# Optimization experiments

Measured on AMD Instinct MI355X. Metric: run time of the kernel, lower is better.

## Reference

```python
import jax, jax.numpy as jnp
import numpy as np
import math

D_MODEL = 1024
N_HEADS = 16
D_K = D_MODEL // N_HEADS


def setup_inputs() -> dict:
    key = jax.random.key(0)
    ks = jax.random.split(key, 5)
    std = math.sqrt(2.0 / (D_MODEL + D_MODEL))
    x = jax.random.normal(ks[0], (2, 2048, D_MODEL), dtype=jnp.float32)
    W_q = jax.random.normal(ks[1], (D_MODEL, D_MODEL), dtype=jnp.float32) * std
    W_k = jax.random.normal(ks[2], (D_MODEL, D_MODEL), dtype=jnp.float32) * std
    W_v = jax.random.normal(ks[3], (D_MODEL, D_MODEL), dtype=jnp.float32) * std
    W_o = jax.random.normal(ks[4], (D_MODEL, D_MODEL), dtype=jnp.float32) * std
    return {"x": x, "W_q": W_q, "W_k": W_k, "W_v": W_v, "W_o": W_o}


def reference(x, W_q, W_k, W_v, W_o):
    B, S, D = x.shape
    H, dk = N_HEADS, D_K
    # projections: (B,S,D) @ (D,D)
    def split_heads(t):  # (B,S,D) -> (B,H,S,dk)
        return t.reshape(B, S, H, dk).transpose(0, 2, 1, 3)
    Q = split_heads(x @ W_q)
    K = split_heads(x @ W_k)
    V = split_heads(x @ W_v)
    scale = 1.0 / math.sqrt(dk)
    scores = jnp.einsum("bhqd,bhkd->bhqk", Q, K) * scale  # (B,H,S,S)
    attn = jax.nn.softmax(scores, axis=-1)
    out = jnp.einsum("bhqk,bhkd->bhqd", attn, V)  # (B,H,S,dk)
    concat = out.transpose(0, 2, 1, 3).reshape(B, S, D)
    return concat @ W_o
```

## Files before the change

kernel.cpp:

```cpp
#include <hip/hip_runtime.h>
#include <hip/hip_bf16.h>
#include <math.h>

#define DMODEL 1024
#define NHEADS 16
#define DKH    64
#define BATCH  2
#define SEQ    2048
#define MROWS  (BATCH * SEQ)
#define LOG2E  1.4426950408889634f

typedef __bf16 bf16_t;
typedef bf16_t bf16x8 __attribute__((ext_vector_type(8)));
typedef bf16_t bf16x4 __attribute__((ext_vector_type(4)));
typedef float  floatx4 __attribute__((ext_vector_type(4)));

__device__ __forceinline__ void glds16(const bf16_t* g, bf16_t* l) {
    __builtin_amdgcn_global_load_lds((__attribute__((address_space(1))) unsigned*)(g),
                                     (__attribute__((address_space(3))) unsigned*)(l),
                                     16, 0, 0);
}

__global__ void prep_kernel(const float* __restrict__ x,
                            const float* __restrict__ W0, const float* __restrict__ W1,
                            const float* __restrict__ W2, const float* __restrict__ W3,
                            bf16_t* __restrict__ xb, bf16_t* __restrict__ Wt) {
    __shared__ float t[32][33];
    int bx = blockIdx.x, by = blockIdx.y, z = blockIdx.z;
    int tx = threadIdx.x, ty = threadIdx.y;
    if (z == 0) {
#pragma unroll
        for (int k = 0; k < 16; ++k) {
            int row = by * 128 + k * 8 + ty;
            int col = bx * 32 + tx;
            xb[(size_t)row * DMODEL + col] = (bf16_t)x[(size_t)row * DMODEL + col];
        }
        return;
    }
    const float* W = (z == 1) ? W0 : (z == 2) ? W1 : (z == 3) ? W2 : W3;
    bf16_t* dst = Wt + (size_t)(z - 1) * DMODEL * DMODEL;
#pragma unroll
    for (int i = 0; i < 32; i += 8)
        t[ty + i][tx] = W[(size_t)(by * 32 + ty + i) * DMODEL + bx * 32 + tx];
    __syncthreads();
#pragma unroll
    for (int i = 0; i < 32; i += 8)
        dst[(size_t)(bx * 32 + ty + i) * DMODEL + by * 32 + tx] = (bf16_t)t[tx][ty + i];
}

__global__ __launch_bounds__(256) void gemm_qkv_kernel(const bf16_t* __restrict__ A,
                                                       const bf16_t* __restrict__ Bt,
                                                       bf16_t* __restrict__ Qb,
                                                       bf16_t* __restrict__ Kfb,
                                                       bf16_t* __restrict__ Vfb) {
    __shared__ bf16_t sm[16384];
    bf16_t* As = sm;
    bf16_t* Bs = sm + 8192;
    int tid = threadIdx.x;
    int w = tid >> 6, l = tid & 63, g = l >> 4, lm = l & 15;
    int wr = w >> 1, wc = w & 1;
    int m0 = blockIdx.y * 128, n0 = blockIdx.x * 128;
    int r8 = l >> 3, s8 = l & 7, cw = s8 ^ r8;

    floatx4 acc[4][4];
#pragma unroll
    for (int i = 0; i < 4; ++i)
#pragma unroll
        for (int j = 0; j < 4; ++j) { floatx4 z = {0.f, 0.f, 0.f, 0.f}; acc[i][j] = z; }

    const bf16_t* Ag = A  + (size_t)(m0 + w * 32 + r8) * DMODEL + cw * 8;
    const bf16_t* Bg = Bt + (size_t)(n0 + w * 32 + r8) * DMODEL + cw * 8;

    for (int k0 = 0; k0 < DMODEL; k0 += 64) {
        __syncthreads();
#pragma unroll
        for (int j = 0; j < 4; ++j) {
            glds16(Ag + (size_t)j * 8 * DMODEL + k0, &As[(w * 32 + j * 8) * 64]);
            glds16(Bg + (size_t)j * 8 * DMODEL + k0, &Bs[(w * 32 + j * 8) * 64]);
        }
        __syncthreads();
#pragma unroll
        for (int kk = 0; kk < 2; ++kk) {
            bf16x8 af[4], bfr[4];
            int c = kk * 4 + g;
            int sw = (c ^ (lm & 7)) * 8;
#pragma unroll
            for (int i = 0; i < 4; ++i) {
                af[i]  = *(const bf16x8*)&As[(wr * 64 + i * 16 + lm) * 64 + sw];
                bfr[i] = *(const bf16x8*)&Bs[(wc * 64 + i * 16 + lm) * 64 + sw];
            }
#pragma unroll
            for (int i = 0; i < 4; ++i)
#pragma unroll
                for (int j = 0; j < 4; ++j)
                    acc[i][j] = __builtin_amdgcn_mfma_f32_16x16x32_bf16(af[i], bfr[j], acc[i][j], 0, 0, 0);
        }
    }

    __syncthreads();
    int mat = n0 >> 10;
    int headb = (n0 & 1023) >> 6;
    int b = m0 >> 11;
    if (mat == 0) {
#pragma unroll
        for (int i = 0; i < 4; ++i)
#pragma unroll
            for (int j = 0; j < 4; ++j) {
                int d = j * 16 + lm;
                int so = wr * 64 + i * 16 + g * 4;
#pragma unroll
                for (int r = 0; r < 4; ++r)
                    sm[wc * 8192 + (so + r) * 64 + d] = (bf16_t)(acc[i][j][r] * (0.125f * LOG2E));
            }
        __syncthreads();
        int sbase = m0 & 2047;
#pragma unroll
        for (int rep = 0; rep < 8; ++rep) {
            int idx = rep * 256 + tid;
            int c = idx >> 10;
            int off = (idx & 1023) * 8;
            bf16_t* dst = Qb + ((size_t)(b * NHEADS + headb + c) * SEQ + sbase) * DKH + off;
            *(bf16x8*)dst = *(const bf16x8*)&sm[c * 8192 + off];
        }
    } else if (mat == 1) {
#pragma unroll
        for (int i = 0; i < 4; ++i)
#pragma unroll
            for (int j = 0; j < 4; ++j) {
                int d = j * 16 + lm;
                int base = (wc * 2 + wr) * 4096 + (i * 2 + (d >> 5)) * 512 + ((d >> 3) & 3) * 128 + (d & 7);
#pragma unroll
                for (int r = 0; r < 4; ++r)
                    sm[base + (g * 4 + r) * 8] = (bf16_t)acc[i][j][r];
            }
        __syncthreads();
        int ktb = (m0 & 2047) >> 6;
#pragma unroll
        for (int rep = 0; rep < 8; ++rep) {
            int idx = rep * 256 + tid;
            int c = idx >> 9;
            int off = (idx & 511) * 8;
            int bh2 = b * NHEADS + headb + (c >> 1);
            int kt = ktb + (c & 1);
            *(bf16x8*)(Kfb + ((size_t)bh2 * 32 + kt) * 4096 + off) = *(const bf16x8*)&sm[c * 4096 + off];
        }
    } else {
#pragma unroll
        for (int i = 0; i < 4; ++i)
#pragma unroll
            for (int j = 0; j < 4; ++j) {
                int base = (wc * 2 + wr) * 4096 + (j * 2 + (i >> 1)) * 512 +
                           (((i & 1) * 2 + (g >> 1)) * 16 + lm) * 8 + (g & 1) * 4;
                bf16x4 pk = {(bf16_t)acc[i][j][0], (bf16_t)acc[i][j][1],
                             (bf16_t)acc[i][j][2], (bf16_t)acc[i][j][3]};
                *(bf16x4*)&sm[base] = pk;
            }
        __syncthreads();
        int ktb = (m0 & 2047) >> 6;
#pragma unroll
        for (int rep = 0; rep < 8; ++rep) {
            int idx = rep * 256 + tid;
            int c = idx >> 9;
            int off = (idx & 511) * 8;
            int bh2 = b * NHEADS + headb + (c >> 1);
            int kt = ktb + (c & 1);
            *(bf16x8*)(Vfb + ((size_t)bh2 * 32 + kt) * 4096 + off) = *(const bf16x8*)&sm[c * 4096 + off];
        }
    }
}

__global__ __launch_bounds__(256) void gemmO_kernel(const bf16_t* __restrict__ A,
                                                    const bf16_t* __restrict__ Bt,
                                                    float* __restrict__ outp) {
    __shared__ bf16_t As[64 * 64];
    __shared__ bf16_t Bs[128 * 64];
    int tid = threadIdx.x;
    int w = tid >> 6, l = tid & 63, g = l >> 4, lm = l & 15;
    int wr = w & 1, wc = w >> 1;
    int m0 = blockIdx.y * 64, n0 = blockIdx.x * 128;
    int r8 = l >> 3, s8 = l & 7, cw = s8 ^ r8;

    floatx4 acc[2][4];
#pragma unroll
    for (int i = 0; i < 2; ++i)
#pragma unroll
        for (int j = 0; j < 4; ++j) { floatx4 z = {0.f, 0.f, 0.f, 0.f}; acc[i][j] = z; }

    const bf16_t* Ag = A  + (size_t)(m0 + w * 16 + r8) * DMODEL + cw * 8;
    const bf16_t* Bg = Bt + (size_t)(n0 + w * 32 + r8) * DMODEL + cw * 8;

    for (int k0 = 0; k0 < DMODEL; k0 += 64) {
        __syncthreads();
#pragma unroll
        for (int j = 0; j < 2; ++j)
            glds16(Ag + (size_t)j * 8 * DMODEL + k0, &As[(w * 16 + j * 8) * 64]);
#pragma unroll
        for (int j = 0; j < 4; ++j)
            glds16(Bg + (size_t)j * 8 * DMODEL + k0, &Bs[(w * 32 + j * 8) * 64]);
        __syncthreads();
#pragma unroll
        for (int kk = 0; kk < 2; ++kk) {
            bf16x8 af[2], bfr[4];
            int c = kk * 4 + g;
            int sw = (c ^ (lm & 7)) * 8;
#pragma unroll
            for (int i = 0; i < 2; ++i)
                af[i] = *(const bf16x8*)&As[(wr * 32 + i * 16 + lm) * 64 + sw];
#pragma unroll
            for (int j = 0; j < 4; ++j)
                bfr[j] = *(const bf16x8*)&Bs[(wc * 64 + j * 16 + lm) * 64 + sw];
#pragma unroll
            for (int i = 0; i < 2; ++i)
#pragma unroll
                for (int j = 0; j < 4; ++j)
                    acc[i][j] = __builtin_amdgcn_mfma_f32_16x16x32_bf16(af[i], bfr[j], acc[i][j], 0, 0, 0);
        }
    }

#pragma unroll
    for (int i = 0; i < 2; ++i)
#pragma unroll
        for (int j = 0; j < 4; ++j) {
            int nc = n0 + wc * 64 + j * 16 + lm;
            int mb = m0 + wr * 32 + i * 16 + g * 4;
#pragma unroll
            for (int r = 0; r < 4; ++r)
                outp[(size_t)(mb + r) * DMODEL + nc] = acc[i][j][r];
        }
}

__global__ __launch_bounds__(256, 2) void attn_kernel(const bf16_t* __restrict__ Q,
                                                      const bf16_t* __restrict__ Kf,
                                                      const bf16_t* __restrict__ Vf,
                                                      bf16_t* __restrict__ Cc) {
    __shared__ __align__(16) char smem[41984];
    bf16_t* Ps   = (bf16_t*)smem;
    float*  Mbuf = (float*)smem;
    float*  Lbuf = (float*)(smem + 36864);
    bf16_t* Ct   = (bf16_t*)(smem + 37888);

    int tid = threadIdx.x;
    int w = tid >> 6, l = tid & 63, g = l >> 4, lm = l & 15;
    int bh = blockIdx.x, b = bh >> 4, h = bh & 15;
    int q0 = blockIdx.y * 64;
    int sw = lm & 6;
    int s1 = sw >> 1;

    const bf16_t* Qh  = Q  + ((size_t)bh * SEQ + q0) * DKH;
    const bf16_t* Kfh = Kf + (size_t)bh * 32 * 4096 + l * 8;
    const bf16_t* Vfh = Vf + (size_t)bh * 32 * 4096 + l * 8;

    bf16x8 qf[4][2];
#pragma unroll
    for (int nt = 0; nt < 4; ++nt)
#pragma unroll
        for (int kk = 0; kk < 2; ++kk)
            qf[nt][kk] = *(const bf16x8*)(Qh + (size_t)(nt * 16 + lm) * DKH + kk * 32 + g * 8);

    floatx4 oacc[4][4];
#pragma unroll
    for (int dt = 0; dt < 4; ++dt)
#pragma unroll
        for (int nt = 0; nt < 4; ++nt) { floatx4 z = {0.f, 0.f, 0.f, 0.f}; oacc[dt][nt] = z; }
    float lsum[4] = {0.f, 0.f, 0.f, 0.f};

    int kt0 = w * 8;
    bf16x8 kfa[2][2], kfb[2][2], vfa[4], vfb[4];
    {
        const bf16_t* Kb0 = Kfh + (size_t)kt0 * 4096;
#pragma unroll
        for (int m2 = 0; m2 < 2; ++m2)
#pragma unroll
            for (int kk = 0; kk < 2; ++kk)
                kfa[m2][kk] = *(const bf16x8*)(Kb0 + (m2 * 2 + kk) * 512);
    }

    for (int it = 0; it < 8; ++it) {
        const bf16_t* Tb = Kfh + (size_t)(kt0 + it) * 4096;
        const bf16_t* Vb = Vfh + (size_t)(kt0 + it) * 4096;
        const bf16_t* Tn = Kfh + (size_t)(kt0 + ((it < 7) ? it + 1 : 0)) * 4096;

#pragma unroll
        for (int dt = 0; dt < 4; ++dt) vfa[dt] = *(const bf16x8*)(Vb + (dt * 2 + 0) * 512);
#pragma unroll
        for (int m2 = 0; m2 < 2; ++m2)
#pragma unroll
            for (int kk = 0; kk < 2; ++kk)
                kfb[m2][kk] = *(const bf16x8*)(Tb + (4 + m2 * 2 + kk) * 512);

        floatx4 sa[2][4];
#pragma unroll
        for (int m2 = 0; m2 < 2; ++m2)
#pragma unroll
            for (int nt = 0; nt < 4; ++nt) { floatx4 z = {0.f, 0.f, 0.f, 0.f}; sa[m2][nt] = z; }
#pragma unroll
        for (int kk = 0; kk < 2; ++kk)
#pragma unroll
            for (int m2 = 0; m2 < 2; ++m2)
#pragma unroll
                for (int nt = 0; nt < 4; ++nt)
                    sa[m2][nt] = __builtin_amdgcn_mfma_f32_16x16x32_bf16(kfa[m2][kk], qf[nt][kk], sa[m2][nt], 0, 0, 0);

#pragma unroll
        for (int dt = 0; dt < 4; ++dt) vfb[dt] = *(const bf16x8*)(Vb + (dt * 2 + 1) * 512);
#pragma unroll
        for (int m2 = 0; m2 < 2; ++m2)
#pragma unroll
            for (int kk = 0; kk < 2; ++kk)
                kfa[m2][kk] = *(const bf16x8*)(Tn + (m2 * 2 + kk) * 512);

        floatx4 sb[2][4];
#pragma unroll
        for (int m2 = 0; m2 < 2; ++m2)
#pragma unroll
            for (int nt = 0; nt < 4; ++nt) { floatx4 z = {0.f, 0.f, 0.f, 0.f}; sb[m2][nt] = z; }
#pragma unroll
        for (int kk = 0; kk < 2; ++kk)
#pragma unroll
            for (int m2 = 0; m2 < 2; ++m2)
#pragma unroll
                for (int nt = 0; nt < 4; ++nt)
                    sb[m2][nt] = __builtin_amdgcn_mfma_f32_16x16x32_bf16(kfb[m2][kk], qf[nt][kk], sb[m2][nt], 0, 0, 0);

#pragma unroll
        for (int m2 = 0; m2 < 2; ++m2)
#pragma unroll
            for (int nt = 0; nt < 4; ++nt) {
                float p0 = __builtin_amdgcn_exp2f(sa[m2][nt][0]);
                float p1 = __builtin_amdgcn_exp2f(sa[m2][nt][1]);
                float p2 = __builtin_amdgcn_exp2f(sa[m2][nt][2]);
                float p3 = __builtin_amdgcn_exp2f(sa[m2][nt][3]);
                lsum[nt] += (p0 + p1) + (p2 + p3);
                bf16x4 pk = {(bf16_t)p0, (bf16_t)p1, (bf16_t)p2, (bf16_t)p3};
                *(bf16x4*)&Ps[w * 2048 + (nt * 16 + lm) * 32 + (((m2 * 4 + g) ^ sw) << 2)] = pk;
            }
        {
            bf16x8 bp[4];
#pragma unroll
            for (int nt = 0; nt < 4; ++nt)
                bp[nt] = *(const bf16x8*)&Ps[w * 2048 + (nt * 16 + lm) * 32 + ((g ^ s1) << 3)];
#pragma unroll
            for (int dt = 0; dt < 4; ++dt)
#pragma unroll
                for (int nt = 0; nt < 4; ++nt)
                    oacc[dt][nt] = __builtin_amdgcn_mfma_f32_16x16x32_bf16(vfa[dt], bp[nt], oacc[dt][nt], 0, 0, 0);
        }

#pragma unroll
        for (int m2 = 0; m2 < 2; ++m2)
#pragma unroll
            for (int nt = 0; nt < 4; ++nt) {
                float p0 = __builtin_amdgcn_exp2f(sb[m2][nt][0]);
                float p1 = __builtin_amdgcn_exp2f(sb[m2][nt][1]);
                float p2 = __builtin_amdgcn_exp2f(sb[m2][nt][2]);
                float p3 = __builtin_amdgcn_exp2f(sb[m2][nt][3]);
                lsum[nt] += (p0 + p1) + (p2 + p3);
                bf16x4 pk = {(bf16_t)p0, (bf16_t)p1, (bf16_t)p2, (bf16_t)p3};
                *(bf16x4*)&Ps[w * 2048 + (nt * 16 + lm) * 32 + (((m2 * 4 + g) ^ sw) << 2)] = pk;
            }
        {
            bf16x8 bp[4];
#pragma unroll
            for (int nt = 0; nt < 4; ++nt)
                bp[nt] = *(const bf16x8*)&Ps[w * 2048 + (nt * 16 + lm) * 32 + ((g ^ s1) << 3)];
#pragma unroll
            for (int dt = 0; dt < 4; ++dt)
#pragma unroll
                for (int nt = 0; nt < 4; ++nt)
                    oacc[dt][nt] = __builtin_amdgcn_mfma_f32_16x16x32_bf16(vfb[dt], bp[nt], oacc[dt][nt], 0, 0, 0);
        }
    }

#pragma unroll
    for (int nt = 0; nt < 4; ++nt) {
        float s = lsum[nt];
        s += __shfl_xor(s, 16, 64);
        s += __shfl_xor(s, 32, 64);
        lsum[nt] = s;
    }

    float linv = 0.f;
#pragma unroll
    for (int p = 0; p < 2; ++p) {
        __syncthreads();
#pragma unroll
        for (int dh = 0; dh < 2; ++dh) {
            int dt = p * 2 + dh;
#pragma unroll
            for (int nt = 0; nt < 4; ++nt)
                *(floatx4*)&Mbuf[w * 2304 + (nt * 16 + lm) * 36 + dh * 16 + g * 4] = oacc[dt][nt];
        }
        if (p == 0 && g == 0)
#pragma unroll
            for (int nt = 0; nt < 4; ++nt)
                Lbuf[w * 64 + nt * 16 + lm] = lsum[nt];
        __syncthreads();
        if (p == 0) {
            float lt = 0.f;
#pragma unroll
            for (int w2 = 0; w2 < 4; ++w2)
                lt += Lbuf[w2 * 64 + w * 16 + lm];
            linv = 1.0f / lt;
        }
#pragma unroll
        for (int cc = 0; cc < 2; ++cc) {
            floatx4 s = {0.f, 0.f, 0.f, 0.f};
#pragma unroll
            for (int w2 = 0; w2 < 4; ++w2)
                s += *(const floatx4*)&Mbuf[w2 * 2304 + (w * 16 + lm) * 36 + cc * 16 + g * 4];
            bf16x4 pk = {(bf16_t)(s[0] * linv), (bf16_t)(s[1] * linv),
                         (bf16_t)(s[2] * linv), (bf16_t)(s[3] * linv)};
            *(bf16x4*)&Ct[w * 512 + lm * 32 + cc * 16 + g * 4] = pk;
        }
        {
            int row = l >> 2, dp = l & 3;
            bf16x8 v = *(const bf16x8*)&Ct[w * 512 + row * 32 + dp * 8];
            *(bf16x8*)&Cc[((size_t)(b * SEQ + q0 + w * 16 + row)) * DMODEL + h * DKH + p * 32 + dp * 8] = v;
        }
    }
}

extern "C" void kernel_launch(void* const* d_in, const int* in_sizes, int n_in,
                              void* d_out, int out_size, void* d_ws, size_t ws_size,
                              hipStream_t stream) {
    const float* x  = (const float*)d_in[0];
    const float* Wq = (const float*)d_in[1];
    const float* Wk = (const float*)d_in[2];
    const float* Wv = (const float*)d_in[3];
    const float* Wo = (const float*)d_in[4];

    const size_t NX = (size_t)MROWS * DMODEL;
    const size_t NW = (size_t)DMODEL * DMODEL;
    bf16_t* ws  = (bf16_t*)d_ws;
    bf16_t* xb  = ws;
    bf16_t* Wt  = xb + NX;
    bf16_t* Wto = Wt + 3 * NW;
    bf16_t* Qb  = Wt + 4 * NW;
    bf16_t* Kfb = Qb + NX;
    bf16_t* Vfb = Kfb + NX;
    bf16_t* Cc  = Vfb + NX;

    prep_kernel<<<dim3(32, 32, 5), dim3(32, 8), 0, stream>>>(x, Wq, Wk, Wv, Wo, xb, Wt);

    gemm_qkv_kernel<<<dim3(3 * DMODEL / 128, MROWS / 128), 256, 0, stream>>>(xb, Wt, Qb, Kfb, Vfb);

    attn_kernel<<<dim3(BATCH * NHEADS, SEQ / 64), 256, 0, stream>>>(Qb, Kfb, Vfb, Cc);

    gemmO_kernel<<<dim3(DMODEL / 128, MROWS / 64), 256, 0, stream>>>(Cc, Wto, (float*)d_out);
}
```

Measured before the change: 177.7 us.

## Store Q in fragment-packed layout, vectorize x conversion, pad P tile instead of XOR swizzle

The QKV GEMM now writes Q in the same MFMA-fragment-packed tile layout already used for K, with the softmax scale folded in. The attention kernel can then load each Q fragment with contiguous per-lane 16-byte loads instead of strided row reads. The x-to-bf16 conversion in the prep kernel now uses float4 loads and bf16x4 stores. The P and C staging buffers in shared memory switch from XOR swizzling to row padding (stride 40), which slightly increases LDS use and may change bank-conflict behaviour.

```diff
diff --git a/kernel.cpp b/kernel.cpp
--- a/kernel.cpp
+++ b/kernel.cpp
@@ -29,11 +29,15 @@
     int bx = blockIdx.x, by = blockIdx.y, z = blockIdx.z;
     int tx = threadIdx.x, ty = threadIdx.y;
     if (z == 0) {
-#pragma unroll
-        for (int k = 0; k < 16; ++k) {
-            int row = by * 128 + k * 8 + ty;
-            int col = bx * 32 + tx;
-            xb[(size_t)row * DMODEL + col] = (bf16_t)x[(size_t)row * DMODEL + col];
+        int tid = ty * 32 + tx;
+#pragma unroll
+        for (int k = 0; k < 4; ++k) {
+            int slot = k * 256 + tid;
+            int row = by * 128 + (slot >> 3);
+            int col = bx * 32 + (slot & 7) * 4;
+            float4 v = *(const float4*)&x[(size_t)row * DMODEL + col];
+            bf16x4 o = {(bf16_t)v.x, (bf16_t)v.y, (bf16_t)v.z, (bf16_t)v.w};
+            *(bf16x4*)&xb[(size_t)row * DMODEL + col] = o;
         }
         return;
     }
@@ -50,7 +54,7 @@
 
 __global__ __launch_bounds__(256) void gemm_qkv_kernel(const bf16_t* __restrict__ A,
                                                        const bf16_t* __restrict__ Bt,
-                                                       bf16_t* __restrict__ Qb,
+                                                       bf16_t* __restrict__ Qfb,
                                                        bf16_t* __restrict__ Kfb,
                                                        bf16_t* __restrict__ Vfb) {
     __shared__ bf16_t sm[16384];
@@ -101,28 +105,10 @@
     int mat = n0 >> 10;
     int headb = (n0 & 1023) >> 6;
     int b = m0 >> 11;
-    if (mat == 0) {
-#pragma unroll
-        for (int i = 0; i < 4; ++i)
-#pragma unroll
-            for (int j = 0; j < 4; ++j) {
-                int d = j * 16 + lm;
-                int so = wr * 64 + i * 16 + g * 4;
-#pragma unroll
-                for (int r = 0; r < 4; ++r)
-                    sm[wc * 8192 + (so + r) * 64 + d] = (bf16_t)(acc[i][j][r] * (0.125f * LOG2E));
-            }
-        __syncthreads();
-        int sbase = m0 & 2047;
-#pragma unroll
-        for (int rep = 0; rep < 8; ++rep) {
-            int idx = rep * 256 + tid;
-            int c = idx >> 10;
-            int off = (idx & 1023) * 8;
-            bf16_t* dst = Qb + ((size_t)(b * NHEADS + headb + c) * SEQ + sbase) * DKH + off;
-            *(bf16x8*)dst = *(const bf16x8*)&sm[c * 8192 + off];
-        }
-    } else if (mat == 1) {
+    int ktb = (m0 & 2047) >> 6;
+    float scale = (mat == 0) ? (0.125f * LOG2E) : 1.0f;
+
+    if (mat <= 1) {
 #pragma unroll
         for (int i = 0; i < 4; ++i)
 #pragma unroll
@@ -131,19 +117,8 @@
                 int base = (wc * 2 + wr) * 4096 + (i * 2 + (d >> 5)) * 512 + ((d >> 3) & 3) * 128 + (d & 7);
 #pragma unroll
                 for (int r = 0; r < 4; ++r)
-                    sm[base + (g * 4 + r) * 8] = (bf16_t)acc[i][j][r];
+                    sm[base + (g * 4 + r) * 8] = (bf16_t)(acc[i][j][r] * scale);
             }
-        __syncthreads();
-        int ktb = (m0 & 2047) >> 6;
-#pragma unroll
-        for (int rep = 0; rep < 8; ++rep) {
-            int idx = rep * 256 + tid;
-            int c = idx >> 9;
-            int off = (idx & 511) * 8;
-            int bh2 = b * NHEADS + headb + (c >> 1);
-            int kt = ktb + (c & 1);
-            *(bf16x8*)(Kfb + ((size_t)bh2 * 32 + kt) * 4096 + off) = *(const bf16x8*)&sm[c * 4096 + off];
-        }
     } else {
 #pragma unroll
         for (int i = 0; i < 4; ++i)
@@ -155,17 +130,17 @@
                              (bf16_t)acc[i][j][2], (bf16_t)acc[i][j][3]};
                 *(bf16x4*)&sm[base] = pk;
             }
-        __syncthreads();
-        int ktb = (m0 & 2047) >> 6;
-#pragma unroll
-        for (int rep = 0; rep < 8; ++rep) {
-            int idx = rep * 256 + tid;
-            int c = idx >> 9;
-            int off = (idx & 511) * 8;
-            int bh2 = b * NHEADS + headb + (c >> 1);
-            int kt = ktb + (c & 1);
-            *(bf16x8*)(Vfb + ((size_t)bh2 * 32 + kt) * 4096 + off) = *(const bf16x8*)&sm[c * 4096 + off];
-        }
+    }
+    __syncthreads();
+    bf16_t* outbuf = (mat == 0) ? Qfb : (mat == 1) ? Kfb : Vfb;
+#pragma unroll
+    for (int rep = 0; rep < 8; ++rep) {
+        int idx = rep * 256 + tid;
+        int c = idx >> 9;
+        int off = (idx & 511) * 8;
+        int bh2 = b * NHEADS + headb + (c >> 1);
+        int kt = ktb + (c & 1);
+        *(bf16x8*)(outbuf + ((size_t)bh2 * 32 + kt) * 4096 + off) = *(const bf16x8*)&sm[c * 4096 + off];
     }
 }
 
@@ -229,11 +204,11 @@
         }
 }
 
-__global__ __launch_bounds__(256, 2) void attn_kernel(const bf16_t* __restrict__ Q,
+__global__ __launch_bounds__(256, 2) void attn_kernel(const bf16_t* __restrict__ Qf,
                                                       const bf16_t* __restrict__ Kf,
                                                       const bf16_t* __restrict__ Vf,
                                                       bf16_t* __restrict__ Cc) {
-    __shared__ __align__(16) char smem[41984];
+    __shared__ __align__(16) char smem[43008];
     bf16_t* Ps   = (bf16_t*)smem;
     float*  Mbuf = (float*)smem;
     float*  Lbuf = (float*)(smem + 36864);
@@ -243,10 +218,8 @@
     int w = tid >> 6, l = tid & 63, g = l >> 4, lm = l & 15;
     int bh = blockIdx.x, b = bh >> 4, h = bh & 15;
     int q0 = blockIdx.y * 64;
-    int sw = lm & 6;
-    int s1 = sw >> 1;
-
-    const bf16_t* Qh  = Q  + ((size_t)bh * SEQ + q0) * DKH;
+
+    const bf16_t* Qfh = Qf + ((size_t)bh * 32 + (q0 >> 6)) * 4096 + l * 8;
     const bf16_t* Kfh = Kf + (size_t)bh * 32 * 4096 + l * 8;
     const bf16_t* Vfh = Vf + (size_t)bh * 32 * 4096 + l * 8;
 
@@ -255,7 +228,7 @@
     for (int nt = 0; nt < 4; ++nt)
 #pragma unroll
         for (int kk = 0; kk < 2; ++kk)
-            qf[nt][kk] = *(const bf16x8*)(Qh + (size_t)(nt * 16 + lm) * DKH + kk * 32 + g * 8);
+            qf[nt][kk] = *(const bf16x8*)(Qfh + (nt * 2 + kk) * 512);
 
     floatx4 oacc[4][4];
 #pragma unroll
@@ -332,13 +305,13 @@
                 float p3 = __builtin_amdgcn_exp2f(sa[m2][nt][3]);
                 lsum[nt] += (p0 + p1) + (p2 + p3);
                 bf16x4 pk = {(bf16_t)p0, (bf16_t)p1, (bf16_t)p2, (bf16_t)p3};
-                *(bf16x4*)&Ps[w * 2048 + (nt * 16 + lm) * 32 + (((m2 * 4 + g) ^ sw) << 2)] = pk;
+                *(bf16x4*)&Ps[w * 2560 + (nt * 16 + lm) * 40 + m2 * 16 + g * 4] = pk;
             }
         {
             bf16x8 bp[4];
 #pragma unroll
             for (int nt = 0; nt < 4; ++nt)
-                bp[nt] = *(const bf16x8*)&Ps[w * 2048 + (nt * 16 + lm) * 32 + ((g ^ s1) << 3)];
+                bp[nt] = *(const bf16x8*)&Ps[w * 2560 + (nt * 16 + lm) * 40 + g * 8];
 #pragma unroll
             for (int dt = 0; dt < 4; ++dt)
 #pragma unroll
@@ -356,13 +329,13 @@
                 float p3 = __builtin_amdgcn_exp2f(sb[m2][nt][3]);
                 lsum[nt] += (p0 + p1) + (p2 + p3);
                 bf16x4 pk = {(bf16_t)p0, (bf16_t)p1, (bf16_t)p2, (bf16_t)p3};
-                *(bf16x4*)&Ps[w * 2048 + (nt * 16 + lm) * 32 + (((m2 * 4 + g) ^ sw) << 2)] = pk;
+                *(bf16x4*)&Ps[w * 2560 + (nt * 16 + lm) * 40 + m2 * 16 + g * 4] = pk;
             }
         {
             bf16x8 bp[4];
 #pragma unroll
             for (int nt = 0; nt < 4; ++nt)
-                bp[nt] = *(const bf16x8*)&Ps[w * 2048 + (nt * 16 + lm) * 32 + ((g ^ s1) << 3)];
+                bp[nt] = *(const bf16x8*)&Ps[w * 2560 + (nt * 16 + lm) * 40 + g * 8];
 #pragma unroll
             for (int dt = 0; dt < 4; ++dt)
 #pragma unroll
@@ -410,11 +383,11 @@
                 s += *(const floatx4*)&Mbuf[w2 * 2304 + (w * 16 + lm) * 36 + cc * 16 + g * 4];
             bf16x4 pk = {(bf16_t)(s[0] * linv), (bf16_t)(s[1] * linv),
                          (bf16_t)(s[2] * linv), (bf16_t)(s[3] * linv)};
-            *(bf16x4*)&Ct[w * 512 + lm * 32 + cc * 16 + g * 4] = pk;
+            *(bf16x4*)&Ct[w * 640 + lm * 40 + cc * 16 + g * 4] = pk;
         }
         {
             int row = l >> 2, dp = l & 3;
-            bf16x8 v = *(const bf16x8*)&Ct[w * 512 + row * 32 + dp * 8];
+            bf16x8 v = *(const bf16x8*)&Ct[w * 640 + row * 40 + dp * 8];
             *(bf16x8*)&Cc[((size_t)(b * SEQ + q0 + w * 16 + row)) * DMODEL + h * DKH + p * 32 + dp * 8] = v;
         }
     }
@@ -435,16 +408,16 @@
     bf16_t* xb  = ws;
     bf16_t* Wt  = xb + NX;
     bf16_t* Wto = Wt + 3 * NW;
-    bf16_t* Qb  = Wt + 4 * NW;
-    bf16_t* Kfb = Qb + NX;
+    bf16_t* Qfb = Wt + 4 * NW;
+    bf16_t* Kfb = Qfb + NX;
     bf16_t* Vfb = Kfb + NX;
     bf16_t* Cc  = Vfb + NX;
 
     prep_kernel<<<dim3(32, 32, 5), dim3(32, 8), 0, stream>>>(x, Wq, Wk, Wv, Wo, xb, Wt);
 
-    gemm_qkv_kernel<<<dim3(3 * DMODEL / 128, MROWS / 128), 256, 0, stream>>>(xb, Wt, Qb, Kfb, Vfb);
-
-    attn_kernel<<<dim3(BATCH * NHEADS, SEQ / 64), 256, 0, stream>>>(Qb, Kfb, Vfb, Cc);
+    gemm_qkv_kernel<<<dim3(3 * DMODEL / 128, MROWS / 128), 256, 0, stream>>>(xb, Wt, Qfb, Kfb, Vfb);
+
+    attn_kernel<<<dim3(BATCH * NHEADS, SEQ / 64), 256, 0, stream>>>(Qfb, Kfb, Vfb, Cc);
 
     gemmO_kernel<<<dim3(DMODEL / 128, MROWS / 64), 256, 0, stream>>>(Cc, Wto, (float*)d_out);
 }
```

New measurement: 175.7 us. About the same (-1.1%).
